# Kernel optimization log

Hardware: AMD Instinct MI355X
Metric: run time of the kernel (lower is better)

The kernel has to match this reference:

```python
import jax, jax.numpy as jnp
import numpy as np

D_MODEL = 1024
N_HEADS = 16
EPS = 1e-5


def setup_inputs() -> dict:
    key = jax.random.key(0)
    ks = jax.random.split(key, 16)
    B, L, D = 2, 2048, D_MODEL
    s = 0.02
    return {
        "x": jax.random.normal(ks[0], (B, L, D), jnp.float32),
        "pad_mask": jnp.ones((B, L), dtype=bool),
        "in_proj_w": jax.random.normal(ks[1], (3 * D, D), jnp.float32) * s,
        "in_proj_b": jnp.zeros((3 * D,), jnp.float32),
        "out_w": jax.random.normal(ks[2], (D, D), jnp.float32) * s,
        "out_b": jnp.zeros((D,), jnp.float32),
        "ln1_g": jnp.ones((D,), jnp.float32),
        "ln1_b": jnp.zeros((D,), jnp.float32),
        "ln2_g": jnp.ones((D,), jnp.float32),
        "ln2_b": jnp.zeros((D,), jnp.float32),
        "w1": jax.random.normal(ks[3], (4 * D, D), jnp.float32) * s,
        "b1": jnp.zeros((4 * D,), jnp.float32),
        "w2": jax.random.normal(ks[4], (D, 4 * D), jnp.float32) * s,
        "b2": jnp.zeros((D,), jnp.float32),
    }


def _layer_norm(x, g, b):
    mu = jnp.mean(x, axis=-1, keepdims=True)
    var = jnp.mean(jnp.square(x - mu), axis=-1, keepdims=True)
    return (x - mu) * jax.lax.rsqrt(var + EPS) * g + b


def reference(x, pad_mask, in_proj_w, in_proj_b, out_w, out_b,
              ln1_g, ln1_b, ln2_g, ln2_b, w1, b1, w2, b2):
    B, L, D = x.shape
    H = N_HEADS
    hd = D // H
    # qkv projection (torch Linear layout: y = x @ W.T + b)
    qkv = x @ in_proj_w.T + in_proj_b  # [B, L, 3D]
    q, k, v = jnp.split(qkv, 3, axis=-1)
    q = q.reshape(B, L, H, hd).transpose(0, 2, 1, 3)  # [B,H,L,hd]
    k = k.reshape(B, L, H, hd).transpose(0, 2, 1, 3)
    v = v.reshape(B, L, H, hd).transpose(0, 2, 1, 3)
    scores = jnp.einsum("bhqd,bhkd->bhqk", q, k) / jnp.sqrt(jnp.asarray(hd, x.dtype))
    # causal + key-padding mask, additive -inf as in the torch module
    causal = jnp.triu(jnp.ones((L, L), dtype=bool), 1)  # True above diag
    masked = causal[None, None, :, :] | (~pad_mask)[:, None, None, :]
    scores = jnp.where(masked, -jnp.inf, scores)
    p = jax.nn.softmax(scores, axis=-1)  # dropout is identity at eval
    attn = jnp.einsum("bhqk,bhkd->bhqd", p, v)
    attn = attn.transpose(0, 2, 1, 3).reshape(B, L, D)
    attn = attn @ out_w.T + out_b
    x = _layer_norm(x + attn, ln1_g, ln1_b)
    h = jax.nn.gelu(x @ w1.T + b1, approximate=False)  # torch GELU default = erf
    ff = h @ w2.T + b2
    x = _layer_norm(x + ff, ln2_g, ln2_b)
    return x
```

## Files before the change

### kernel.cpp

```cpp
#include <hip/hip_runtime.h>
#include <cstdint>
#include <cstddef>

#define D_MODEL 1024
#define B_SZ 2
#define L_SEQ 2048
#define M_TOK (B_SZ * L_SEQ)
#define H_HEADS 16
#define HD 64
#define D3 (3 * D_MODEL)
#define D4 (4 * D_MODEL)

typedef unsigned short u16;
typedef __attribute__((ext_vector_type(8))) short short8;
typedef __attribute__((ext_vector_type(4))) short short4v;
typedef __attribute__((ext_vector_type(4))) float f32x4;

static __device__ __forceinline__ u16 f2bf(float f) {
    uint32_t x = __float_as_uint(f);
    x += 0x7fffu + ((x >> 16) & 1u);
    return (u16)(x >> 16);
}

static __device__ __forceinline__ void gll16(const void* g, void* s) {
    __builtin_amdgcn_global_load_lds((const __attribute__((address_space(1))) void*)g,
                                     (__attribute__((address_space(3))) void*)s, 16, 0, 0);
}

__global__ __launch_bounds__(256) void cvt_kernel(const float* __restrict__ in,
                                                  u16* __restrict__ out, int n4) {
    int i = blockIdx.x * 256 + threadIdx.x;
    if (i < n4) {
        f32x4 v = *(const f32x4*)&in[(size_t)i * 4];
        short4v o;
        o[0] = (short)f2bf(v[0]); o[1] = (short)f2bf(v[1]);
        o[2] = (short)f2bf(v[2]); o[3] = (short)f2bf(v[3]);
        *(short4v*)&out[(size_t)i * 4] = o;
    }
}

template <int EPI>
__global__ __launch_bounds__(256) void gemm_bt(const u16* __restrict__ A, const u16* __restrict__ Bm,
                                               const float* __restrict__ bias,
                                               const float* __restrict__ resid,
                                               float* __restrict__ outf, u16* __restrict__ outb,
                                               int M, int N, int K) {
    __shared__ __align__(16) u16 As[128 * 32];
    __shared__ __align__(16) u16 Bs[128 * 32];
    const int tid = threadIdx.x;
    const int w = tid >> 6, l = tid & 63, g = l >> 4, c = l & 15;
    const int wm = w >> 1, wn = w & 1;
    const int m0 = blockIdx.y * 128, n0 = blockIdx.x * 128;

    f32x4 acc[4][4];
#pragma unroll
    for (int i = 0; i < 4; i++)
#pragma unroll
        for (int j = 0; j < 4; j++) acc[i][j] = (f32x4){0.f, 0.f, 0.f, 0.f};

    for (int kt = 0; kt < K; kt += 32) {
#pragma unroll
        for (int rep = 0; rep < 2; rep++) {
            int chb = w * 128 + rep * 64;
            int ch = chb + l;
            int row = ch >> 2, q = ch & 3;
            gll16(A + (size_t)(m0 + row) * K + kt + q * 8, &As[chb * 8]);
            gll16(Bm + (size_t)(n0 + row) * K + kt + q * 8, &Bs[chb * 8]);
        }
        __syncthreads();
        short8 af[4], bfv[4];
#pragma unroll
        for (int mi = 0; mi < 4; mi++)
            af[mi] = *(const short8*)&As[(wm * 64 + mi * 16 + c) * 32 + g * 8];
#pragma unroll
        for (int ni = 0; ni < 4; ni++)
            bfv[ni] = *(const short8*)&Bs[(wn * 64 + ni * 16 + c) * 32 + g * 8];
#pragma unroll
        for (int mi = 0; mi < 4; mi++)
#pragma unroll
            for (int ni = 0; ni < 4; ni++)
                acc[mi][ni] = __builtin_amdgcn_mfma_f32_16x16x32_bf16(af[mi], bfv[ni], acc[mi][ni], 0, 0, 0);
        __syncthreads();
    }

#pragma unroll
    for (int mi = 0; mi < 4; mi++)
#pragma unroll
        for (int ni = 0; ni < 4; ni++)
#pragma unroll
            for (int r = 0; r < 4; r++) {
                int row = m0 + wm * 64 + mi * 16 + g * 4 + r;
                int col = n0 + wn * 64 + ni * 16 + c;
                float v = acc[mi][ni][r] + bias[col];
                size_t o = (size_t)row * N + col;
                if constexpr (EPI == 0) {
                    outb[o] = f2bf(v);
                } else if constexpr (EPI == 1) {
                    outf[o] = v + resid[o];
                } else {
                    v = 0.5f * v * (1.0f + erff(v * 0.70710678118654752f));
                    outb[o] = f2bf(v);
                }
            }
}

template <bool WB>
__global__ __launch_bounds__(256) void ln_kernel(const float* __restrict__ in,
                                                 const float* __restrict__ gw, const float* __restrict__ bw,
                                                 float* __restrict__ outf, u16* __restrict__ outb) {
    __shared__ float red[8];
    const int row = blockIdx.x;
    const int t = threadIdx.x;
    const float* p = in + (size_t)row * D_MODEL;
    f32x4 v = *(const f32x4*)&p[t * 4];
    float s1 = v[0] + v[1] + v[2] + v[3];
    float s2 = v[0] * v[0] + v[1] * v[1] + v[2] * v[2] + v[3] * v[3];
#pragma unroll
    for (int m = 32; m >= 1; m >>= 1) {
        s1 += __shfl_xor(s1, m, 64);
        s2 += __shfl_xor(s2, m, 64);
    }
    int w = t >> 6;
    if ((t & 63) == 0) { red[w] = s1; red[4 + w] = s2; }
    __syncthreads();
    s1 = red[0] + red[1] + red[2] + red[3];
    s2 = red[4] + red[5] + red[6] + red[7];
    float mu = s1 * (1.0f / D_MODEL);
    float var = s2 * (1.0f / D_MODEL) - mu * mu;
    float rs = rsqrtf(var + 1e-5f);
    int col = t * 4;
    f32x4 gg = *(const f32x4*)&gw[col];
    f32x4 bb = *(const f32x4*)&bw[col];
    f32x4 o;
#pragma unroll
    for (int j = 0; j < 4; j++) o[j] = (v[j] - mu) * rs * gg[j] + bb[j];
    *(f32x4*)&outf[(size_t)row * D_MODEL + col] = o;
    if constexpr (WB) {
        short4v ob;
#pragma unroll
        for (int j = 0; j < 4; j++) ob[j] = (short)f2bf(o[j]);
        *(short4v*)&outb[(size_t)row * D_MODEL + col] = ob;
    }
}

__global__ __launch_bounds__(256) void attn_kernel(const u16* __restrict__ qkv, u16* __restrict__ attnout) {
    __shared__ __align__(16) u16 Kt[64 * 64];
    __shared__ __align__(16) u16 Vt[64 * 64];
    __shared__ __align__(16) u16 Pp[4][16 * 64];

    const int qb = blockIdx.x;
    const int bh = blockIdx.y;
    const int b = bh >> 4, h = bh & 15;
    const int tid = threadIdx.x;
    const int w = tid >> 6, l = tid & 63, g = l >> 4, c = l & 15;

    short8 qf[2];
    {
        int qr = qb * 64 + w * 16 + c;
        size_t base = (size_t)(b * L_SEQ + qr) * D3 + h * HD;
        qf[0] = *(const short8*)&qkv[base + g * 8];
        qf[1] = *(const short8*)&qkv[base + 32 + g * 8];
    }

    f32x4 o_acc[4];
#pragma unroll
    for (int i = 0; i < 4; i++) o_acc[i] = (f32x4){0.f, 0.f, 0.f, 0.f};
    float mrow[4] = {-1e30f, -1e30f, -1e30f, -1e30f};
    float lsum[4] = {0.f, 0.f, 0.f, 0.f};

    for (int kt = 0; kt <= qb; kt++) {
#pragma unroll
        for (int rep = 0; rep < 2; rep++) {
            int chb = w * 128 + rep * 64;
            int ch = chb + l;
            int kk = ch >> 3, j = ch & 7;
            int jj = j ^ (kk & 7);
            gll16(&qkv[(size_t)(b * L_SEQ + kt * 64 + kk) * D3 + D_MODEL + h * HD + jj * 8], &Kt[chb * 8]);
        }
        {
            int kk0 = (tid & 31) * 2;
            int d0 = (tid >> 5) * 8;
            const u16* vsrc = &qkv[(size_t)(b * L_SEQ + kt * 64 + kk0) * D3 + 2 * D_MODEL + h * HD + d0];
            short8 v0 = *(const short8*)vsrc;
            short8 v1 = *(const short8*)(vsrc + D3);
#pragma unroll
            for (int jd = 0; jd < 8; jd++) {
                int d = d0 + jd;
                int byte_off = (d * 128 + kk0 * 2) ^ ((d & 7) << 4);
                uint32_t pack = ((uint32_t)(u16)v0[jd]) | (((uint32_t)(u16)v1[jd]) << 16);
                *(uint32_t*)((char*)Vt + byte_off) = pack;
            }
        }
        __syncthreads();

        f32x4 s_acc[4];
#pragma unroll
        for (int f = 0; f < 4; f++) s_acc[f] = (f32x4){0.f, 0.f, 0.f, 0.f};
#pragma unroll
        for (int f = 0; f < 4; f++) {
            int kkcol = f * 16 + c;
#pragma unroll
            for (int s = 0; s < 2; s++) {
                int byte_off = (kkcol * 128 + (s * 32 + g * 8) * 2) ^ ((kkcol & 7) << 4);
                short8 kf = *(const short8*)((const char*)Kt + byte_off);
                s_acc[f] = __builtin_amdgcn_mfma_f32_16x16x32_bf16(qf[s], kf, s_acc[f], 0, 0, 0);
            }
        }

        float p[4][4];
#pragma unroll
        for (int r = 0; r < 4; r++) {
            int qr_l = g * 4 + r;
            int qr_g = qb * 64 + w * 16 + qr_l;
            float mx = -1e30f;
#pragma unroll
            for (int f = 0; f < 4; f++) {
                float sv = s_acc[f][r] * 0.125f;
                int kk_g = kt * 64 + f * 16 + c;
                if (kk_g > qr_g) sv = -1e30f;
                p[f][r] = sv;
                mx = fmaxf(mx, sv);
            }
            mx = fmaxf(mx, __shfl_xor(mx, 1, 64));
            mx = fmaxf(mx, __shfl_xor(mx, 2, 64));
            mx = fmaxf(mx, __shfl_xor(mx, 4, 64));
            mx = fmaxf(mx, __shfl_xor(mx, 8, 64));
            float mnew = fmaxf(mrow[r], mx);
            float al = __expf(mrow[r] - mnew);
            float ps = 0.f;
#pragma unroll
            for (int f = 0; f < 4; f++) {
                float e = __expf(p[f][r] - mnew);
                p[f][r] = e;
                ps += e;
            }
            ps += __shfl_xor(ps, 1, 64);
            ps += __shfl_xor(ps, 2, 64);
            ps += __shfl_xor(ps, 4, 64);
            ps += __shfl_xor(ps, 8, 64);
            lsum[r] = lsum[r] * al + ps;
            mrow[r] = mnew;
#pragma unroll
            for (int df = 0; df < 4; df++) o_acc[df][r] *= al;
        }

        {
            char* pb = (char*)&Pp[w][0];
#pragma unroll
            for (int r = 0; r < 4; r++) {
                int qr_l = g * 4 + r;
#pragma unroll
                for (int f = 0; f < 4; f++) {
                    int byte_off = (qr_l * 128 + (f * 16 + c) * 2) ^ ((qr_l & 7) << 4);
                    *(u16*)(pb + byte_off) = f2bf(p[f][r]);
                }
            }
        }

#pragma unroll
        for (int s = 0; s < 2; s++) {
            int pbyte = (c * 128 + (s * 32 + g * 8) * 2) ^ ((c & 7) << 4);
            short8 pf = *(const short8*)((const char*)&Pp[w][0] + pbyte);
#pragma unroll
            for (int df = 0; df < 4; df++) {
                int d = df * 16 + c;
                int vbyte = (d * 128 + (s * 32 + g * 8) * 2) ^ ((d & 7) << 4);
                short8 vf = *(const short8*)((const char*)Vt + vbyte);
                o_acc[df] = __builtin_amdgcn_mfma_f32_16x16x32_bf16(pf, vf, o_acc[df], 0, 0, 0);
            }
        }
        __syncthreads();
    }

#pragma unroll
    for (int df = 0; df < 4; df++)
#pragma unroll
        for (int r = 0; r < 4; r++) {
            int tok = b * L_SEQ + qb * 64 + w * 16 + g * 4 + r;
            int col = h * HD + df * 16 + c;
            attnout[(size_t)tok * D_MODEL + col] = f2bf(o_acc[df][r] / lsum[r]);
        }
}

extern "C" void kernel_launch(void* const* d_in, const int* in_sizes, int n_in,
                              void* d_out, int out_size, void* d_ws, size_t ws_size,
                              hipStream_t stream) {
    const float* x     = (const float*)d_in[0];
    const float* in_w  = (const float*)d_in[2];
    const float* in_b  = (const float*)d_in[3];
    const float* out_w = (const float*)d_in[4];
    const float* out_b = (const float*)d_in[5];
    const float* ln1_g = (const float*)d_in[6];
    const float* ln1_b = (const float*)d_in[7];
    const float* ln2_g = (const float*)d_in[8];
    const float* ln2_b = (const float*)d_in[9];
    const float* w1    = (const float*)d_in[10];
    const float* b1    = (const float*)d_in[11];
    const float* w2    = (const float*)d_in[12];
    const float* b2    = (const float*)d_in[13];
    float* out = (float*)d_out;

    char* ws = (char*)d_ws;
    size_t off = 0;
    auto alloc = [&](size_t bytes) {
        char* p = ws + off;
        off += (bytes + 255) & ~(size_t)255;
        return p;
    };
    u16* wqkv_b = (u16*)alloc((size_t)D3 * D_MODEL * 2);
    u16* wout_b = (u16*)alloc((size_t)D_MODEL * D_MODEL * 2);
    u16* w1_b   = (u16*)alloc((size_t)D4 * D_MODEL * 2);
    u16* w2_b   = (u16*)alloc((size_t)D_MODEL * D4 * 2);
    u16* xb     = (u16*)alloc((size_t)M_TOK * D_MODEL * 2);
    u16* qkv_b  = (u16*)alloc((size_t)M_TOK * D3 * 2);
    u16* attnb  = (u16*)alloc((size_t)M_TOK * D_MODEL * 2);
    float* x1f  = (float*)alloc((size_t)M_TOK * D_MODEL * 4);
    u16* x1b    = (u16*)alloc((size_t)M_TOK * D_MODEL * 2);
    u16* hb     = (u16*)alloc((size_t)M_TOK * D4 * 2);
    float* res1 = (float*)qkv_b;
    float* res2 = (float*)qkv_b;

    auto cvt = [&](const float* src, u16* dst, size_t n) {
        int n4 = (int)(n / 4);
        cvt_kernel<<<(n4 + 255) / 256, 256, 0, stream>>>(src, dst, n4);
    };
    cvt(in_w, wqkv_b, (size_t)D3 * D_MODEL);
    cvt(out_w, wout_b, (size_t)D_MODEL * D_MODEL);
    cvt(w1, w1_b, (size_t)D4 * D_MODEL);
    cvt(w2, w2_b, (size_t)D_MODEL * D4);
    cvt(x, xb, (size_t)M_TOK * D_MODEL);

    gemm_bt<0><<<dim3(D3 / 128, M_TOK / 128), 256, 0, stream>>>(
        xb, wqkv_b, in_b, nullptr, nullptr, qkv_b, M_TOK, D3, D_MODEL);
    attn_kernel<<<dim3(L_SEQ / 64, B_SZ * H_HEADS), 256, 0, stream>>>(qkv_b, attnb);
    gemm_bt<1><<<dim3(D_MODEL / 128, M_TOK / 128), 256, 0, stream>>>(
        attnb, wout_b, out_b, x, res1, nullptr, M_TOK, D_MODEL, D_MODEL);
    ln_kernel<true><<<M_TOK, 256, 0, stream>>>(res1, ln1_g, ln1_b, x1f, x1b);
    gemm_bt<2><<<dim3(D4 / 128, M_TOK / 128), 256, 0, stream>>>(
        x1b, w1_b, b1, nullptr, nullptr, hb, M_TOK, D4, D_MODEL);
    gemm_bt<1><<<dim3(D_MODEL / 128, M_TOK / 128), 256, 0, stream>>>(
        hb, w2_b, b2, x1f, res2, nullptr, M_TOK, D_MODEL, D4);
    ln_kernel<false><<<M_TOK, 256, 0, stream>>>(res2, ln2_g, ln2_b, out, nullptr);
}
```

Measured before the change: 505.5 us.

## Write QKV in head-major layout with pre-transposed V; load attention operands directly from global

The QKV GEMM epilogue now scatters Q and K into per-head [B,H,L,64] buffers and V into a transposed [B,H,64,L] buffer. The attention kernel drops its LDS staging of K and V and the in-kernel V transpose, loading MFMA fragments straight from global memory. Each wave now handles 32 query rows (128 per block), which doubles reuse of the K/V fragments. Query tiles are launched heaviest-first to balance the causal work. The costs are scattered, uncoalesced stores in the GEMM epilogue (especially the transposed V) and redundant global reads across waves that used to share LDS.

```diff
diff --git a/kernel.cpp b/kernel.cpp
--- a/kernel.cpp
+++ b/kernel.cpp
@@ -44,6 +44,7 @@
                                                const float* __restrict__ bias,
                                                const float* __restrict__ resid,
                                                float* __restrict__ outf, u16* __restrict__ outb,
+                                               u16* __restrict__ outb2, u16* __restrict__ outb3,
                                                int M, int N, int K) {
     __shared__ __align__(16) u16 As[128 * 32];
     __shared__ __align__(16) u16 Bs[128 * 32];
@@ -97,9 +98,23 @@
                     outb[o] = f2bf(v);
                 } else if constexpr (EPI == 1) {
                     outf[o] = v + resid[o];
-                } else {
+                } else if constexpr (EPI == 2) {
                     v = 0.5f * v * (1.0f + erff(v * 0.70710678118654752f));
                     outb[o] = f2bf(v);
+                } else {
+                    int bb = row >> 11, ll = row & 2047;
+                    int d = col & 63;
+                    u16 bv = f2bf(v);
+                    if (col < 1024) {
+                        int h = col >> 6;
+                        outb[((size_t)((bb * 16 + h) * 2048 + ll)) * 64 + d] = bv;
+                    } else if (col < 2048) {
+                        int h = (col - 1024) >> 6;
+                        outb2[((size_t)((bb * 16 + h) * 2048 + ll)) * 64 + d] = bv;
+                    } else {
+                        int h = (col - 2048) >> 6;
+                        outb3[((size_t)((bb * 16 + h) * 64 + d)) * 2048 + ll] = bv;
+                    }
                 }
             }
 }
@@ -143,109 +158,106 @@
     }
 }
 
-__global__ __launch_bounds__(256) void attn_kernel(const u16* __restrict__ qkv, u16* __restrict__ attnout) {
-    __shared__ __align__(16) u16 Kt[64 * 64];
-    __shared__ __align__(16) u16 Vt[64 * 64];
-    __shared__ __align__(16) u16 Pp[4][16 * 64];
-
-    const int qb = blockIdx.x;
+__global__ __launch_bounds__(256) void attn_kernel(const u16* __restrict__ Qh,
+                                                   const u16* __restrict__ Kh,
+                                                   const u16* __restrict__ Vt,
+                                                   u16* __restrict__ attnout) {
+    __shared__ __align__(16) u16 Pp[4][2][16 * 64];
+
     const int bh = blockIdx.y;
-    const int b = bh >> 4, h = bh & 15;
+    const int qt = (int)gridDim.x - 1 - (int)blockIdx.x;
     const int tid = threadIdx.x;
     const int w = tid >> 6, l = tid & 63, g = l >> 4, c = l & 15;
-
-    short8 qf[2];
-    {
-        int qr = qb * 64 + w * 16 + c;
-        size_t base = (size_t)(b * L_SEQ + qr) * D3 + h * HD;
-        qf[0] = *(const short8*)&qkv[base + g * 8];
-        qf[1] = *(const short8*)&qkv[base + 32 + g * 8];
-    }
-
-    f32x4 o_acc[4];
-#pragma unroll
-    for (int i = 0; i < 4; i++) o_acc[i] = (f32x4){0.f, 0.f, 0.f, 0.f};
-    float mrow[4] = {-1e30f, -1e30f, -1e30f, -1e30f};
-    float lsum[4] = {0.f, 0.f, 0.f, 0.f};
-
-    for (int kt = 0; kt <= qb; kt++) {
-#pragma unroll
-        for (int rep = 0; rep < 2; rep++) {
-            int chb = w * 128 + rep * 64;
-            int ch = chb + l;
-            int kk = ch >> 3, j = ch & 7;
-            int jj = j ^ (kk & 7);
-            gll16(&qkv[(size_t)(b * L_SEQ + kt * 64 + kk) * D3 + D_MODEL + h * HD + jj * 8], &Kt[chb * 8]);
+    const int r0 = qt * 128 + w * 32;
+    const u16* Qb = Qh + (size_t)bh * L_SEQ * HD;
+    const u16* Kb = Kh + (size_t)bh * L_SEQ * HD;
+    const u16* Vb = Vt + (size_t)bh * HD * L_SEQ;
+
+    short8 qf[2][2];
+#pragma unroll
+    for (int qi = 0; qi < 2; qi++)
+#pragma unroll
+        for (int s = 0; s < 2; s++)
+            qf[qi][s] = *(const short8*)&Qb[(size_t)(r0 + qi * 16 + c) * HD + s * 32 + g * 8];
+
+    f32x4 o_acc[2][4];
+    float mrow[2][4], lsum[2][4];
+#pragma unroll
+    for (int qi = 0; qi < 2; qi++)
+#pragma unroll
+        for (int i = 0; i < 4; i++) {
+            o_acc[qi][i] = (f32x4){0.f, 0.f, 0.f, 0.f};
+            mrow[qi][i] = -1e30f;
+            lsum[qi][i] = 0.f;
         }
-        {
-            int kk0 = (tid & 31) * 2;
-            int d0 = (tid >> 5) * 8;
-            const u16* vsrc = &qkv[(size_t)(b * L_SEQ + kt * 64 + kk0) * D3 + 2 * D_MODEL + h * HD + d0];
-            short8 v0 = *(const short8*)vsrc;
-            short8 v1 = *(const short8*)(vsrc + D3);
-#pragma unroll
-            for (int jd = 0; jd < 8; jd++) {
-                int d = d0 + jd;
-                int byte_off = (d * 128 + kk0 * 2) ^ ((d & 7) << 4);
-                uint32_t pack = ((uint32_t)(u16)v0[jd]) | (((uint32_t)(u16)v1[jd]) << 16);
-                *(uint32_t*)((char*)Vt + byte_off) = pack;
-            }
-        }
-        __syncthreads();
-
-        f32x4 s_acc[4];
-#pragma unroll
-        for (int f = 0; f < 4; f++) s_acc[f] = (f32x4){0.f, 0.f, 0.f, 0.f};
-#pragma unroll
-        for (int f = 0; f < 4; f++) {
-            int kkcol = f * 16 + c;
-#pragma unroll
-            for (int s = 0; s < 2; s++) {
-                int byte_off = (kkcol * 128 + (s * 32 + g * 8) * 2) ^ ((kkcol & 7) << 4);
-                short8 kf = *(const short8*)((const char*)Kt + byte_off);
-                s_acc[f] = __builtin_amdgcn_mfma_f32_16x16x32_bf16(qf[s], kf, s_acc[f], 0, 0, 0);
-            }
-        }
-
-        float p[4][4];
-#pragma unroll
-        for (int r = 0; r < 4; r++) {
-            int qr_l = g * 4 + r;
-            int qr_g = qb * 64 + w * 16 + qr_l;
-            float mx = -1e30f;
-#pragma unroll
-            for (int f = 0; f < 4; f++) {
-                float sv = s_acc[f][r] * 0.125f;
-                int kk_g = kt * 64 + f * 16 + c;
-                if (kk_g > qr_g) sv = -1e30f;
-                p[f][r] = sv;
-                mx = fmaxf(mx, sv);
-            }
-            mx = fmaxf(mx, __shfl_xor(mx, 1, 64));
-            mx = fmaxf(mx, __shfl_xor(mx, 2, 64));
-            mx = fmaxf(mx, __shfl_xor(mx, 4, 64));
-            mx = fmaxf(mx, __shfl_xor(mx, 8, 64));
-            float mnew = fmaxf(mrow[r], mx);
-            float al = __expf(mrow[r] - mnew);
-            float ps = 0.f;
-#pragma unroll
-            for (int f = 0; f < 4; f++) {
-                float e = __expf(p[f][r] - mnew);
-                p[f][r] = e;
-                ps += e;
-            }
-            ps += __shfl_xor(ps, 1, 64);
-            ps += __shfl_xor(ps, 2, 64);
-            ps += __shfl_xor(ps, 4, 64);
-            ps += __shfl_xor(ps, 8, 64);
-            lsum[r] = lsum[r] * al + ps;
-            mrow[r] = mnew;
-#pragma unroll
-            for (int df = 0; df < 4; df++) o_acc[df][r] *= al;
-        }
-
-        {
-            char* pb = (char*)&Pp[w][0];
+
+    const int ktmax = (r0 + 31) >> 6;
+    for (int kt = 0; kt <= ktmax; kt++) {
+        short8 kf[4][2];
+#pragma unroll
+        for (int f = 0; f < 4; f++)
+#pragma unroll
+            for (int s = 0; s < 2; s++)
+                kf[f][s] = *(const short8*)&Kb[(size_t)(kt * 64 + f * 16 + c) * HD + s * 32 + g * 8];
+
+        f32x4 s_acc[2][4];
+#pragma unroll
+        for (int qi = 0; qi < 2; qi++)
+#pragma unroll
+            for (int f = 0; f < 4; f++) s_acc[qi][f] = (f32x4){0.f, 0.f, 0.f, 0.f};
+#pragma unroll
+        for (int qi = 0; qi < 2; qi++)
+#pragma unroll
+            for (int f = 0; f < 4; f++)
+#pragma unroll
+                for (int s = 0; s < 2; s++)
+                    s_acc[qi][f] = __builtin_amdgcn_mfma_f32_16x16x32_bf16(qf[qi][s], kf[f][s], s_acc[qi][f], 0, 0, 0);
+
+        short8 vf[4][2];
+#pragma unroll
+        for (int df = 0; df < 4; df++)
+#pragma unroll
+            for (int s = 0; s < 2; s++)
+                vf[df][s] = *(const short8*)&Vb[(size_t)(df * 16 + c) * L_SEQ + kt * 64 + s * 32 + g * 8];
+
+#pragma unroll
+        for (int qi = 0; qi < 2; qi++) {
+            float p[4][4];
+#pragma unroll
+            for (int r = 0; r < 4; r++) {
+                int qr_g = r0 + qi * 16 + g * 4 + r;
+                float mx = -1e30f;
+#pragma unroll
+                for (int f = 0; f < 4; f++) {
+                    float sv = s_acc[qi][f][r] * 0.125f;
+                    int kk_g = kt * 64 + f * 16 + c;
+                    if (kk_g > qr_g) sv = -1e30f;
+                    p[f][r] = sv;
+                    mx = fmaxf(mx, sv);
+                }
+                mx = fmaxf(mx, __shfl_xor(mx, 1, 64));
+                mx = fmaxf(mx, __shfl_xor(mx, 2, 64));
+                mx = fmaxf(mx, __shfl_xor(mx, 4, 64));
+                mx = fmaxf(mx, __shfl_xor(mx, 8, 64));
+                float mnew = fmaxf(mrow[qi][r], mx);
+                float al = __expf(mrow[qi][r] - mnew);
+                float ps = 0.f;
+#pragma unroll
+                for (int f = 0; f < 4; f++) {
+                    float e = __expf(p[f][r] - mnew);
+                    p[f][r] = e;
+                    ps += e;
+                }
+                ps += __shfl_xor(ps, 1, 64);
+                ps += __shfl_xor(ps, 2, 64);
+                ps += __shfl_xor(ps, 4, 64);
+                ps += __shfl_xor(ps, 8, 64);
+                lsum[qi][r] = lsum[qi][r] * al + ps;
+                mrow[qi][r] = mnew;
+#pragma unroll
+                for (int df = 0; df < 4; df++) o_acc[qi][df][r] *= al;
+            }
+            char* pb = (char*)&Pp[w][qi][0];
 #pragma unroll
             for (int r = 0; r < 4; r++) {
                 int qr_l = g * 4 + r;
@@ -257,29 +269,34 @@
             }
         }
 
-#pragma unroll
-        for (int s = 0; s < 2; s++) {
-            int pbyte = (c * 128 + (s * 32 + g * 8) * 2) ^ ((c & 7) << 4);
-            short8 pf = *(const short8*)((const char*)&Pp[w][0] + pbyte);
-#pragma unroll
-            for (int df = 0; df < 4; df++) {
-                int d = df * 16 + c;
-                int vbyte = (d * 128 + (s * 32 + g * 8) * 2) ^ ((d & 7) << 4);
-                short8 vf = *(const short8*)((const char*)Vt + vbyte);
-                o_acc[df] = __builtin_amdgcn_mfma_f32_16x16x32_bf16(pf, vf, o_acc[df], 0, 0, 0);
-            }
-        }
-        __syncthreads();
-    }
-
-#pragma unroll
-    for (int df = 0; df < 4; df++)
-#pragma unroll
-        for (int r = 0; r < 4; r++) {
-            int tok = b * L_SEQ + qb * 64 + w * 16 + g * 4 + r;
-            int col = h * HD + df * 16 + c;
-            attnout[(size_t)tok * D_MODEL + col] = f2bf(o_acc[df][r] / lsum[r]);
-        }
+        asm volatile("s_waitcnt lgkmcnt(0)" ::: "memory");
+        __builtin_amdgcn_sched_barrier(0);
+
+#pragma unroll
+        for (int qi = 0; qi < 2; qi++)
+#pragma unroll
+            for (int s = 0; s < 2; s++) {
+                int pbyte = (c * 128 + (s * 32 + g * 8) * 2) ^ ((c & 7) << 4);
+                short8 pf = *(const short8*)((const char*)&Pp[w][qi][0] + pbyte);
+#pragma unroll
+                for (int df = 0; df < 4; df++)
+                    o_acc[qi][df] = __builtin_amdgcn_mfma_f32_16x16x32_bf16(pf, vf[df][s], o_acc[qi][df], 0, 0, 0);
+            }
+        asm volatile("s_waitcnt lgkmcnt(0)" ::: "memory");
+        __builtin_amdgcn_sched_barrier(0);
+    }
+
+    const int b = bh >> 4, h = bh & 15;
+#pragma unroll
+    for (int qi = 0; qi < 2; qi++)
+#pragma unroll
+        for (int df = 0; df < 4; df++)
+#pragma unroll
+            for (int r = 0; r < 4; r++) {
+                int tok = b * L_SEQ + r0 + qi * 16 + g * 4 + r;
+                int col = h * HD + df * 16 + c;
+                attnout[(size_t)tok * D_MODEL + col] = f2bf(o_acc[qi][df][r] / lsum[qi][r]);
+            }
 }
 
 extern "C" void kernel_launch(void* const* d_in, const int* in_sizes, int n_in,
@@ -312,13 +329,15 @@
     u16* w1_b   = (u16*)alloc((size_t)D4 * D_MODEL * 2);
     u16* w2_b   = (u16*)alloc((size_t)D_MODEL * D4 * 2);
     u16* xb     = (u16*)alloc((size_t)M_TOK * D_MODEL * 2);
-    u16* qkv_b  = (u16*)alloc((size_t)M_TOK * D3 * 2);
+    u16* qh_b   = (u16*)alloc((size_t)M_TOK * D_MODEL * 2);
+    u16* kh_b   = (u16*)alloc((size_t)M_TOK * D_MODEL * 2);
+    u16* vt_b   = (u16*)alloc((size_t)M_TOK * D_MODEL * 2);
     u16* attnb  = (u16*)alloc((size_t)M_TOK * D_MODEL * 2);
     float* x1f  = (float*)alloc((size_t)M_TOK * D_MODEL * 4);
     u16* x1b    = (u16*)alloc((size_t)M_TOK * D_MODEL * 2);
     u16* hb     = (u16*)alloc((size_t)M_TOK * D4 * 2);
-    float* res1 = (float*)qkv_b;
-    float* res2 = (float*)qkv_b;
+    float* res1 = (float*)qh_b;
+    float* res2 = (float*)qh_b;
 
     auto cvt = [&](const float* src, u16* dst, size_t n) {
         int n4 = (int)(n / 4);
@@ -330,15 +349,15 @@
     cvt(w2, w2_b, (size_t)D_MODEL * D4);
     cvt(x, xb, (size_t)M_TOK * D_MODEL);
 
-    gemm_bt<0><<<dim3(D3 / 128, M_TOK / 128), 256, 0, stream>>>(
-        xb, wqkv_b, in_b, nullptr, nullptr, qkv_b, M_TOK, D3, D_MODEL);
-    attn_kernel<<<dim3(L_SEQ / 64, B_SZ * H_HEADS), 256, 0, stream>>>(qkv_b, attnb);
+    gemm_bt<3><<<dim3(D3 / 128, M_TOK / 128), 256, 0, stream>>>(
+        xb, wqkv_b, in_b, nullptr, nullptr, qh_b, kh_b, vt_b, M_TOK, D3, D_MODEL);
+    attn_kernel<<<dim3(L_SEQ / 128, B_SZ * H_HEADS), 256, 0, stream>>>(qh_b, kh_b, vt_b, attnb);
     gemm_bt<1><<<dim3(D_MODEL / 128, M_TOK / 128), 256, 0, stream>>>(
-        attnb, wout_b, out_b, x, res1, nullptr, M_TOK, D_MODEL, D_MODEL);
+        attnb, wout_b, out_b, x, res1, nullptr, nullptr, nullptr, M_TOK, D_MODEL, D_MODEL);
     ln_kernel<true><<<M_TOK, 256, 0, stream>>>(res1, ln1_g, ln1_b, x1f, x1b);
     gemm_bt<2><<<dim3(D4 / 128, M_TOK / 128), 256, 0, stream>>>(
-        x1b, w1_b, b1, nullptr, nullptr, hb, M_TOK, D4, D_MODEL);
+        x1b, w1_b, b1, nullptr, nullptr, hb, nullptr, nullptr, M_TOK, D4, D_MODEL);
     gemm_bt<1><<<dim3(D_MODEL / 128, M_TOK / 128), 256, 0, stream>>>(
-        hb, w2_b, b2, x1f, res2, nullptr, M_TOK, D_MODEL, D4);
+        hb, w2_b, b2, x1f, res2, nullptr, nullptr, nullptr, M_TOK, D_MODEL, D4);
     ln_kernel<false><<<M_TOK, 256, 0, stream>>>(res2, ln2_g, ln2_b, out, nullptr);
 }
```

New measurement: 491.4 us. 2.8% less time.
